# Optimization experiments

Measured on AMD Instinct MI355X. Metric: run time of the kernel, lower is better.

The kernel has to match this reference:

```python
import jax, jax.numpy as jnp
import numpy as np


def setup_inputs() -> dict:
    key = jax.random.key(0)
    k1, k2 = jax.random.split(key)
    B, H, W, D = 4096, 64, 64, 512
    inputs = jax.random.normal(k1, (B, D), dtype=jnp.float32)
    # keras 'random_uniform' initializer default range [-0.05, 0.05]
    weights_map = jax.random.uniform(k2, (H, W, D), dtype=jnp.float32,
                                     minval=-0.05, maxval=0.05)
    return {"inputs": inputs, "weights_map": weights_map}


def reference(inputs, weights_map):
    # inputs: (B, D); weights_map: (H, W, D)
    H, W, D = weights_map.shape
    flat_w = weights_map.reshape(-1, D)              # (N, D), N = H*W
    # avoids materializing the (B, N, D) difference tensor)
    x_sq = jnp.sum(inputs * inputs, axis=1, keepdims=True)    # (B, 1)
    w_sq = jnp.sum(flat_w * flat_w, axis=1)                   # (N,)
    sq_dist = x_sq - 2.0 * (inputs @ flat_w.T) + w_sq         # (B, N)
    sq_dist = jnp.maximum(sq_dist, 0.0)
    bmu_flat = jnp.argmin(sq_dist, axis=1)                    # (B,)
    bmu_y = (bmu_flat // W).astype(jnp.int32)
    bmu_x = (bmu_flat % W).astype(jnp.int32)
    bmu_indices = jnp.stack([bmu_y, bmu_x], axis=1)           # (B, 2)
    min_sq = jnp.take_along_axis(sq_dist, bmu_flat[:, None], axis=1)[:, 0]
    quantization_errors = jnp.sqrt(min_sq)                    # (B,)
    return bmu_indices, quantization_errors
```

## Files before the change

### kernel.cpp

```cpp
#include <hip/hip_runtime.h>

#define B_ROWS 4096
#define N_COLS 4096
#define DIM    512
#define LDK    1024

typedef __attribute__((ext_vector_type(8))) short short8;
typedef __attribute__((ext_vector_type(4))) float floatx4;

__device__ __forceinline__ unsigned short f2bf_rn(float f) {
    unsigned u = __float_as_uint(f);
    u += 0x7fffu + ((u >> 16) & 1u);
    return (unsigned short)(u >> 16);
}
__device__ __forceinline__ float bf2f(unsigned short h) {
    return __uint_as_float(((unsigned)h) << 16);
}

__device__ __forceinline__ unsigned long long pack_key(float v, int idx) {
    unsigned u = __float_as_uint(v);
    u = (u & 0x80000000u) ? ~u : (u | 0x80000000u);
    return ((unsigned long long)u << 32) | (unsigned)idx;
}

__device__ __forceinline__ void async16(const unsigned short* g, unsigned short* l) {
    __builtin_amdgcn_global_load_lds(
        (__attribute__((address_space(1))) void*)g,
        (__attribute__((address_space(3))) void*)l, 16, 0, 0);
}

__global__ __launch_bounds__(256) void som_convert(
    const float* __restrict__ X, const float* __restrict__ Wt,
    unsigned short* __restrict__ Xc, unsigned short* __restrict__ Wc,
    float* __restrict__ x_sq, float* __restrict__ w_sq,
    unsigned long long* __restrict__ packed)
{
    int wave = threadIdx.x >> 6, lane = threadIdx.x & 63;
    int grow = blockIdx.x * 4 + wave;
    bool isX = grow < B_ROWS;
    const float* src = isX ? (X + (size_t)grow * DIM)
                           : (Wt + (size_t)(grow - B_ROWS) * DIM);
    const float4* p4 = (const float4*)src;
    float4 a = p4[lane * 2], b = p4[lane * 2 + 1];
    float f[8] = {a.x, a.y, a.z, a.w, b.x, b.y, b.z, b.w};
    unsigned short hi[8], lo[8];
    float s = 0.f;
    #pragma unroll
    for (int t = 0; t < 8; ++t) {
        hi[t] = f2bf_rn(f[t]);
        lo[t] = f2bf_rn(f[t] - bf2f(hi[t]));
        s = fmaf(f[t], f[t], s);
    }
    unsigned short* dst = (isX ? Xc + (size_t)grow * LDK
                               : Wc + (size_t)(grow - B_ROWS) * LDK) + lane * 8;
    *(ushort4*)(dst)       = make_ushort4(hi[0], hi[1], hi[2], hi[3]);
    *(ushort4*)(dst + 4)   = make_ushort4(hi[4], hi[5], hi[6], hi[7]);
    *(ushort4*)(dst + 512) = make_ushort4(lo[0], lo[1], lo[2], lo[3]);
    *(ushort4*)(dst + 516) = make_ushort4(lo[4], lo[5], lo[6], lo[7]);
    #pragma unroll
    for (int off = 32; off >= 1; off >>= 1) s += __shfl_xor(s, off, 64);
    if (lane == 0) {
        if (isX) { x_sq[grow] = s; packed[grow] = ~0ull; }
        else     { w_sq[grow - B_ROWS] = s; }
    }
}

__global__ __launch_bounds__(256, 3) void som_dist_bf16(
    const unsigned short* __restrict__ Xc, const unsigned short* __restrict__ Wc,
    const float* __restrict__ w_sq, unsigned long long* __restrict__ packed)
{
    __shared__ unsigned short As[128 * 32];
    __shared__ unsigned short Bs[128 * 32];
    const int tid  = threadIdx.x;
    const int wave = tid >> 6, lane = tid & 63;
    const int wr = wave >> 1, wc = wave & 1;
    const int bm = blockIdx.y, bn = blockIdx.x;
    const int quad = lane >> 4, t16 = lane & 15;

    const int srow = lane >> 2;
    const int scol = (lane & 3) * 8;
    const unsigned short* gA = Xc + (size_t)(bm * 128 + wave * 32 + srow) * LDK + scol;
    const unsigned short* gB = Wc + (size_t)(bn * 128 + wave * 32 + srow) * LDK + scol;
    unsigned short* lA0 = &As[(wave * 32 + 0)  * 32];
    unsigned short* lA1 = &As[(wave * 32 + 16) * 32];
    unsigned short* lB0 = &Bs[(wave * 32 + 0)  * 32];
    unsigned short* lB1 = &Bs[(wave * 32 + 16) * 32];

    const unsigned short* pa = &As[(wr * 64 + t16) * 32 + quad * 8];
    const unsigned short* pb = &Bs[(wc * 64 + t16) * 32 + quad * 8];

    floatx4 acc[4][4];
    #pragma unroll
    for (int i = 0; i < 4; ++i)
        #pragma unroll
        for (int j = 0; j < 4; ++j) acc[i][j] = (floatx4){0.f, 0.f, 0.f, 0.f};

    const int aoffs[3] = {0, 0, 512};
    const int boffs[3] = {0, 512, 0};

    #pragma unroll 1
    for (int p = 0; p < 3; ++p) {
        const unsigned short* gAp = gA + aoffs[p];
        const unsigned short* gBp = gB + boffs[p];
        #pragma unroll 1
        for (int k0 = 0; k0 < DIM; k0 += 32) {
            __syncthreads();
            async16(gAp + k0,            lA0);
            async16(gAp + k0 + 16 * LDK, lA1);
            async16(gBp + k0,            lB0);
            async16(gBp + k0 + 16 * LDK, lB1);
            __syncthreads();
            short8 a[4], b[4];
            #pragma unroll
            for (int i = 0; i < 4; ++i) a[i] = *(const short8*)(pa + i * 16 * 32);
            #pragma unroll
            for (int j = 0; j < 4; ++j) b[j] = *(const short8*)(pb + j * 16 * 32);
            #pragma unroll
            for (int i = 0; i < 4; ++i)
                #pragma unroll
                for (int j = 0; j < 4; ++j)
                    acc[i][j] = __builtin_amdgcn_mfma_f32_16x16x32_bf16(
                        a[i], b[j], acc[i][j], 0, 0, 0);
        }
    }

    const int col0 = bn * 128 + wc * 64 + t16;
    float wq[4];
    #pragma unroll
    for (int j = 0; j < 4; ++j) wq[j] = w_sq[col0 + j * 16];
    const int row_base = bm * 128 + wr * 64 + quad * 4;
    #pragma unroll
    for (int i = 0; i < 4; ++i) {
        #pragma unroll
        for (int r = 0; r < 4; ++r) {
            unsigned long long best = ~0ull;
            #pragma unroll
            for (int j = 0; j < 4; ++j) {
                float val = fmaf(-2.f, acc[i][j][r], wq[j]);
                unsigned long long key = pack_key(val, col0 + j * 16);
                best = (key < best) ? key : best;
            }
            #pragma unroll
            for (int m = 1; m <= 8; m <<= 1) {
                unsigned long long o = __shfl_xor(best, m, 64);
                best = (o < best) ? o : best;
            }
            if (t16 == 0)
                atomicMin(&packed[row_base + i * 16 + r], best);
        }
    }
}

__global__ __launch_bounds__(256) void som_finalize(
    const unsigned long long* __restrict__ packed,
    const float* __restrict__ x_sq, float* __restrict__ out)
{
    int b = blockIdx.x * 256 + threadIdx.x;
    unsigned long long p = packed[b];
    unsigned idx = (unsigned)(p & 0xffffffffull);
    unsigned key = (unsigned)(p >> 32);
    unsigned u = (key & 0x80000000u) ? (key & 0x7fffffffu) : ~key;
    float val = __uint_as_float(u);
    float sq = fmaxf(x_sq[b] + val, 0.f);
    out[2 * b]     = (float)(idx >> 6);
    out[2 * b + 1] = (float)(idx & 63);
    out[2 * B_ROWS + b] = sqrtf(sq);
}

extern "C" void kernel_launch(void* const* d_in, const int* in_sizes, int n_in,
                              void* d_out, int out_size, void* d_ws, size_t ws_size,
                              hipStream_t stream) {
    const float* X  = (const float*)d_in[0];
    const float* Wt = (const float*)d_in[1];
    float* out = (float*)d_out;

    unsigned long long* packed = (unsigned long long*)d_ws;
    float* x_sq = (float*)((char*)d_ws + (32 << 10));
    float* w_sq = (float*)((char*)d_ws + (48 << 10));
    unsigned short* Xc = (unsigned short*)((char*)d_ws + (64 << 10));
    unsigned short* Wc = (unsigned short*)((char*)d_ws + (64 << 10) + ((size_t)B_ROWS * LDK * 2));

    som_convert<<<dim3((B_ROWS + N_COLS) / 4), dim3(256), 0, stream>>>(
        X, Wt, Xc, Wc, x_sq, w_sq, packed);
    som_dist_bf16<<<dim3(N_COLS / 128, B_ROWS / 128), dim3(256), 0, stream>>>(
        Xc, Wc, w_sq, packed);
    som_finalize<<<dim3(B_ROWS / 256), dim3(256), 0, stream>>>(packed, x_sq, out);
}
```

Measured before the change: 130.3 us.

## Fuse three bf16 split passes into one K loop reusing hi fragments

Replaces the three separate K sweeps (hi*hi, hi*lo, lo*hi) with a single sweep that loads hi and lo tiles of both operands together, reusing the hi fragments across all three MFMA groups. This cuts the number of barriers and global-to-LDS load rounds by a factor of three and avoids reloading the hi fragments. In exchange it doubles the LDS footprint, which may lower occupancy, and it raises register pressure.

```diff
diff --git a/kernel.cpp b/kernel.cpp
--- a/kernel.cpp
+++ b/kernel.cpp
@@ -69,8 +69,10 @@
     const unsigned short* __restrict__ Xc, const unsigned short* __restrict__ Wc,
     const float* __restrict__ w_sq, unsigned long long* __restrict__ packed)
 {
-    __shared__ unsigned short As[128 * 32];
-    __shared__ unsigned short Bs[128 * 32];
+    __shared__ unsigned short Ah[128 * 32];
+    __shared__ unsigned short Al[128 * 32];
+    __shared__ unsigned short Bh[128 * 32];
+    __shared__ unsigned short Bl[128 * 32];
     const int tid  = threadIdx.x;
     const int wave = tid >> 6, lane = tid & 63;
     const int wr = wave >> 1, wc = wave & 1;
@@ -79,15 +81,19 @@
 
     const int srow = lane >> 2;
     const int scol = (lane & 3) * 8;
-    const unsigned short* gA = Xc + (size_t)(bm * 128 + wave * 32 + srow) * LDK + scol;
-    const unsigned short* gB = Wc + (size_t)(bn * 128 + wave * 32 + srow) * LDK + scol;
-    unsigned short* lA0 = &As[(wave * 32 + 0)  * 32];
-    unsigned short* lA1 = &As[(wave * 32 + 16) * 32];
-    unsigned short* lB0 = &Bs[(wave * 32 + 0)  * 32];
-    unsigned short* lB1 = &Bs[(wave * 32 + 16) * 32];
-
-    const unsigned short* pa = &As[(wr * 64 + t16) * 32 + quad * 8];
-    const unsigned short* pb = &Bs[(wc * 64 + t16) * 32 + quad * 8];
+    const unsigned short* gAh = Xc + (size_t)(bm * 128 + wave * 32 + srow) * LDK + scol;
+    const unsigned short* gBh = Wc + (size_t)(bn * 128 + wave * 32 + srow) * LDK + scol;
+    const unsigned short* gAl = gAh + 512;
+    const unsigned short* gBl = gBh + 512;
+    unsigned short* lAh = &Ah[(wave * 32) * 32];
+    unsigned short* lAl = &Al[(wave * 32) * 32];
+    unsigned short* lBh = &Bh[(wave * 32) * 32];
+    unsigned short* lBl = &Bl[(wave * 32) * 32];
+
+    const unsigned short* pah = &Ah[(wr * 64 + t16) * 32 + quad * 8];
+    const unsigned short* pal = &Al[(wr * 64 + t16) * 32 + quad * 8];
+    const unsigned short* pbh = &Bh[(wc * 64 + t16) * 32 + quad * 8];
+    const unsigned short* pbl = &Bl[(wc * 64 + t16) * 32 + quad * 8];
 
     floatx4 acc[4][4];
     #pragma unroll
@@ -95,33 +101,48 @@
         #pragma unroll
         for (int j = 0; j < 4; ++j) acc[i][j] = (floatx4){0.f, 0.f, 0.f, 0.f};
 
-    const int aoffs[3] = {0, 0, 512};
-    const int boffs[3] = {0, 512, 0};
-
     #pragma unroll 1
-    for (int p = 0; p < 3; ++p) {
-        const unsigned short* gAp = gA + aoffs[p];
-        const unsigned short* gBp = gB + boffs[p];
-        #pragma unroll 1
-        for (int k0 = 0; k0 < DIM; k0 += 32) {
-            __syncthreads();
-            async16(gAp + k0,            lA0);
-            async16(gAp + k0 + 16 * LDK, lA1);
-            async16(gBp + k0,            lB0);
-            async16(gBp + k0 + 16 * LDK, lB1);
-            __syncthreads();
-            short8 a[4], b[4];
-            #pragma unroll
-            for (int i = 0; i < 4; ++i) a[i] = *(const short8*)(pa + i * 16 * 32);
-            #pragma unroll
-            for (int j = 0; j < 4; ++j) b[j] = *(const short8*)(pb + j * 16 * 32);
-            #pragma unroll
-            for (int i = 0; i < 4; ++i)
-                #pragma unroll
-                for (int j = 0; j < 4; ++j)
-                    acc[i][j] = __builtin_amdgcn_mfma_f32_16x16x32_bf16(
-                        a[i], b[j], acc[i][j], 0, 0, 0);
-        }
+    for (int k0 = 0; k0 < DIM; k0 += 32) {
+        __syncthreads();
+        async16(gAh + k0,            lAh);
+        async16(gAh + k0 + 16 * LDK, lAh + 16 * 32);
+        async16(gAl + k0,            lAl);
+        async16(gAl + k0 + 16 * LDK, lAl + 16 * 32);
+        async16(gBh + k0,            lBh);
+        async16(gBh + k0 + 16 * LDK, lBh + 16 * 32);
+        async16(gBl + k0,            lBl);
+        async16(gBl + k0 + 16 * LDK, lBl + 16 * 32);
+        __syncthreads();
+
+        short8 ah[4], bh[4], x[4];
+        #pragma unroll
+        for (int i = 0; i < 4; ++i) ah[i] = *(const short8*)(pah + i * 16 * 32);
+        #pragma unroll
+        for (int j = 0; j < 4; ++j) bh[j] = *(const short8*)(pbh + j * 16 * 32);
+        #pragma unroll
+        for (int i = 0; i < 4; ++i)
+            #pragma unroll
+            for (int j = 0; j < 4; ++j)
+                acc[i][j] = __builtin_amdgcn_mfma_f32_16x16x32_bf16(
+                    ah[i], bh[j], acc[i][j], 0, 0, 0);
+
+        #pragma unroll
+        for (int j = 0; j < 4; ++j) x[j] = *(const short8*)(pbl + j * 16 * 32);
+        #pragma unroll
+        for (int i = 0; i < 4; ++i)
+            #pragma unroll
+            for (int j = 0; j < 4; ++j)
+                acc[i][j] = __builtin_amdgcn_mfma_f32_16x16x32_bf16(
+                    ah[i], x[j], acc[i][j], 0, 0, 0);
+
+        #pragma unroll
+        for (int i = 0; i < 4; ++i) x[i] = *(const short8*)(pal + i * 16 * 32);
+        #pragma unroll
+        for (int i = 0; i < 4; ++i)
+            #pragma unroll
+            for (int j = 0; j < 4; ++j)
+                acc[i][j] = __builtin_amdgcn_mfma_f32_16x16x32_bf16(
+                    x[i], bh[j], acc[i][j], 0, 0, 0);
     }
 
     const int col0 = bn * 128 + wc * 64 + t16;
```

Measured after the change: 123.4 us. 1.06x faster.
